# Kernel optimization log

Hardware: AMD Instinct MI355X
Metric: run time of the kernel (lower is better)

## Reference

```python
import jax, jax.numpy as jnp
import numpy as np

GRID = 128          # grid_size n
C_MARKERS = 32      # marker embed dim C
M_RHS = 64          # number of right-hand sides m
LENGTH_SCALE = 5.0  # spatial Matern length scale
KERNEL_JITTER = 0.01
MARKER_JITTER = 0.01


def _matern15_eigh(n, length_scale):
    # 1D Matern nu=1.5 kernel on linspace(0,1,n), eigendecomposed (as in __init__)
    x = np.linspace(0.0, 1.0, n)
    d = np.abs(x[:, None] - x[None, :]) / length_scale
    s3d = np.sqrt(3.0) * d
    K = (1.0 + s3d) * np.exp(-s3d)
    lam, V = np.linalg.eigh(K)
    return lam.astype(np.float32), V.astype(np.float32)


def setup_inputs() -> dict:
    key = jax.random.key(0)
    k_v, k_e = jax.random.split(key)
    n, C, m = GRID, C_MARKERS, M_RHS

    lam, V = _matern15_eigh(n, LENGTH_SCALE)

    # Marker covariance K_C = E E^T + marker_jitter * I, eigendecomposed
    E = np.asarray(jax.random.normal(k_e, (C, C), dtype=jnp.float32))
    K_C = E @ E.T + MARKER_JITTER * np.eye(C, dtype=np.float32)
    lam_C, V_C = np.linalg.eigh(K_C)

    # triple_eigs[i,j,k] = lam[i]*lam[j]*lam_C[k] + kernel_jitter  (all > 0)
    triple_eigs = (lam[:, None, None] * lam[None, :, None] * lam_C[None, None, :]
                   + KERNEL_JITTER).astype(np.float32)

    v = jax.random.normal(k_v, (n * n * C, m), dtype=jnp.float32)
    return {
        "v": v,
        "V_C": jnp.asarray(V_C.astype(np.float32)),
        "V": jnp.asarray(V),
        "triple_eigs": jnp.asarray(triple_eigs),
    }


def reference(v, V_C, V, triple_eigs):
    """A^{-1} v via triple-Kronecker eigenbasis: 3 forward rotations,
    eigenvalue divide, 3 reverse rotations. v: [n*n*C, m]."""
    n = V.shape[0]
    C = V_C.shape[0]
    m = v.shape[-1]
    V3 = v.reshape(n, n, C, m)
    tmp = jnp.einsum('ijcm,ck->ijkm', V3, V_C)     # rotate marker axis
    tmp = jnp.einsum('ijkm,jb->ibkm', tmp, V)      # rotate spatial y
    tmp = jnp.einsum('ibkm,ia->abkm', tmp, V)      # rotate spatial x
    tmp = tmp / triple_eigs[..., None]             # divide by eigenvalues
    tmp = jnp.einsum('abkm,jb->ajkm', tmp, V)      # un-rotate spatial y
    tmp = jnp.einsum('ajkm,ia->ijkm', tmp, V)      # un-rotate spatial x
    tmp = jnp.einsum('ijkm,ck->ijcm', tmp, V_C)    # un-rotate marker axis
    return tmp.reshape(n * n * C, m)
```

## Files before the change

kernel.cpp:

```cpp
#include <hip/hip_runtime.h>
#include <stdint.h>


typedef unsigned short ushort_t;
typedef __attribute__((ext_vector_type(8))) short short8;
typedef __attribute__((ext_vector_type(4))) float f32x4;

__device__ __forceinline__ ushort_t f2bf(float f) {
  union { float f; uint32_t u; } v; v.f = f;
  uint32_t u = v.u;
  return (ushort_t)((u + 0x7fffu + ((u >> 16) & 1u)) >> 16);
}
__device__ __forceinline__ uint32_t pk2(float a, float b) {
  return (uint32_t)f2bf(a) | ((uint32_t)f2bf(b) << 16);
}
__device__ __forceinline__ float bf2f(ushort_t u) {
  union { uint32_t x; float f; } v; v.x = (uint32_t)u << 16; return v.f;
}

__global__ __launch_bounds__(256) void prep_kernel(
    const float* __restrict__ te, const float* __restrict__ Vg,
    float* __restrict__ rte, ushort_t* __restrict__ Vhg, ushort_t* __restrict__ Vtg) {
  int b = blockIdx.x, t = threadIdx.x;
  if (b < 256) {
    int id = b * 256 + t;
    int o0 = id * 8;
    int k = o0 >> 14, ab0 = o0 & 16383;
    float r[8];
    #pragma unroll
    for (int e = 0; e < 8; ++e) r[e] = 1.0f / te[(ab0 + e) * 32 + k];
    *(float4*)(rte + o0)     = make_float4(r[0], r[1], r[2], r[3]);
    *(float4*)(rte + o0 + 4) = make_float4(r[4], r[5], r[6], r[7]);
  } else {
    int base = (b - 256) * 4096 + t;
    #pragma unroll
    for (int e = 0; e < 16; ++e) {
      int idx = base + e * 256;
      ushort_t us = f2bf(Vg[idx]);
      Vhg[idx] = us;
      Vtg[(idx & 127) * 128 + (idx >> 7)] = us;
    }
  }
}

__global__ __launch_bounds__(256) void k1_rot_t(
    const float* __restrict__ v, const float* __restrict__ VC, ushort_t* __restrict__ W) {
  __shared__ ushort_t Xs[32 * 520];
  __shared__ ushort_t Wt[512 * 32];
  __shared__ float VCs[1024];
  int t = threadIdx.x, bid = blockIdx.x;
  int jc = bid >> 2, mt = bid & 3;
  int ji0 = jc * 32, mm0 = mt * 16;

  #pragma unroll
  for (int e = 0; e < 4; ++e) VCs[e * 256 + t] = VC[e * 256 + t];

  #pragma unroll
  for (int e = 0; e < 4; ++e) {
    int q = e * 256 + t;
    int jj = q >> 5, c = q & 31;
    const float* src = v + (size_t)(ji0 + jj) * 2048 + c * 64 + mm0;
    float4 f0 = *(const float4*)(src);
    float4 f1 = *(const float4*)(src + 4);
    float4 f2 = *(const float4*)(src + 8);
    float4 f3 = *(const float4*)(src + 12);
    uint4 lo = make_uint4(pk2(f0.x, f0.y), pk2(f0.z, f0.w), pk2(f1.x, f1.y), pk2(f1.z, f1.w));
    uint4 hi = make_uint4(pk2(f2.x, f2.y), pk2(f2.z, f2.w), pk2(f3.x, f3.y), pk2(f3.z, f3.w));
    ushort_t* dst = &Xs[jj * 520 + c * 16];
    *(uint4*)dst = lo;
    *(uint4*)(dst + 8) = hi;
  }
  __syncthreads();

  int jj = t & 31, kq = t >> 5;
  float acc[4][16];
  #pragma unroll
  for (int e = 0; e < 4; ++e)
    #pragma unroll
    for (int q = 0; q < 16; ++q) acc[e][q] = 0.f;

  for (int c = 0; c < 32; ++c) {
    const ushort_t* xp = &Xs[jj * 520 + c * 16];
    short8 x0 = *(const short8*)xp;
    short8 x1 = *(const short8*)(xp + 8);
    float vc0 = VCs[c * 32 + kq * 4 + 0];
    float vc1 = VCs[c * 32 + kq * 4 + 1];
    float vc2 = VCs[c * 32 + kq * 4 + 2];
    float vc3 = VCs[c * 32 + kq * 4 + 3];
    #pragma unroll
    for (int q = 0; q < 8; ++q) {
      float xf = bf2f((ushort_t)x0[q]);
      acc[0][q] += vc0 * xf; acc[1][q] += vc1 * xf;
      acc[2][q] += vc2 * xf; acc[3][q] += vc3 * xf;
    }
    #pragma unroll
    for (int q = 0; q < 8; ++q) {
      float xf = bf2f((ushort_t)x1[q]);
      acc[0][8 + q] += vc0 * xf; acc[1][8 + q] += vc1 * xf;
      acc[2][8 + q] += vc2 * xf; acc[3][8 + q] += vc3 * xf;
    }
  }

  #pragma unroll
  for (int e = 0; e < 4; ++e)
    #pragma unroll
    for (int q = 0; q < 16; ++q)
      Wt[((kq * 4 + e) * 16 + q) * 32 + jj] = f2bf(acc[e][q]);
  __syncthreads();

  int part = t & 3, rq = t >> 2;
  #pragma unroll
  for (int e = 0; e < 8; ++e) {
    int row = e * 64 + rq;
    int k = row >> 4, mmi = row & 15;
    uint4 d = *(const uint4*)&Wt[row * 32 + part * 8];
    *(uint4*)(W + (size_t)(k * 64 + mm0 + mmi) * 16384 + ji0 + part * 8) = d;
  }
}

__device__ __forceinline__ void gemm128(const ushort_t (*__restrict__ Am)[136],
                                        const ushort_t (*__restrict__ Bm)[136],
                                        int r0, int c0, int lr, int lk, f32x4 acc[2][4]) {
  #pragma unroll
  for (int fr = 0; fr < 2; ++fr)
    #pragma unroll
    for (int fc = 0; fc < 4; ++fc) acc[fr][fc] = (f32x4){0.f, 0.f, 0.f, 0.f};
  #pragma unroll
  for (int kb = 0; kb < 4; ++kb) {
    short8 a[2], b[4];
    #pragma unroll
    for (int fr = 0; fr < 2; ++fr)
      a[fr] = *(const short8*)&Am[r0 + fr * 16 + lr][kb * 32 + lk];
    #pragma unroll
    for (int fc = 0; fc < 4; ++fc)
      b[fc] = *(const short8*)&Bm[c0 + fc * 16 + lr][kb * 32 + lk];
    #pragma unroll
    for (int fr = 0; fr < 2; ++fr)
      #pragma unroll
      for (int fc = 0; fc < 4; ++fc)
        acc[fr][fc] = __builtin_amdgcn_mfma_f32_16x16x32_bf16(a[fr], b[fc], acc[fr][fc], 0, 0, 0);
  }
}

__global__ __launch_bounds__(512, 2) void k3_chain(
    const ushort_t* __restrict__ W, const ushort_t* __restrict__ Vhg,
    const ushort_t* __restrict__ Vtg, const float* __restrict__ rte,
    ushort_t* __restrict__ U) {
  __shared__ ushort_t Ab[128][136];
  __shared__ ushort_t Vb[128][136];
  int t = threadIdx.x;
  int blk = blockIdx.x;
  int kk = blk >> 6;

  {
    const uint4* Wp = (const uint4*)W + (size_t)blk * 2048;
    const uint4* Vp = (const uint4*)Vtg;
    #pragma unroll
    for (int e = 0; e < 4; ++e) {
      int idx = e * 512 + t;
      int row = idx >> 4, part = idx & 15;
      *(uint4*)&Ab[row][part * 8] = Wp[idx];
      *(uint4*)&Vb[row][part * 8] = Vp[idx];
    }
  }
  __syncthreads();

  int wave = t >> 6, lane = t & 63;
  int r0 = (wave >> 1) * 32, c0 = (wave & 1) * 64;
  int lr = lane & 15;
  int lk = (lane >> 4) * 8;
  int rowreg = (lane >> 4) * 4;

  f32x4 acc[2][4];

  gemm128(Vb, Ab, r0, c0, lr, lk, acc);
  __syncthreads();
  #pragma unroll
  for (int fr = 0; fr < 2; ++fr)
    #pragma unroll
    for (int fc = 0; fc < 4; ++fc)
      #pragma unroll
      for (int r = 0; r < 4; ++r)
        Ab[r0 + fr * 16 + rowreg + r][c0 + fc * 16 + lr] = f2bf(acc[fr][fc][r]);
  __syncthreads();

  gemm128(Ab, Vb, r0, c0, lr, lk, acc);
  #pragma unroll
  for (int fr = 0; fr < 2; ++fr)
    #pragma unroll
    for (int fc = 0; fc < 4; ++fc)
      #pragma unroll
      for (int r = 0; r < 4; ++r) {
        int a = r0 + fr * 16 + rowreg + r;
        int bcol = c0 + fc * 16 + lr;
        acc[fr][fc][r] *= rte[(size_t)kk * 16384 + a * 128 + bcol];
      }
  __syncthreads();
  #pragma unroll
  for (int fr = 0; fr < 2; ++fr)
    #pragma unroll
    for (int fc = 0; fc < 4; ++fc) {
      int bcol = c0 + fc * 16 + lr;
      int abase = r0 + fr * 16 + rowreg;
      uint32_t lo = (uint32_t)f2bf(acc[fr][fc][0]) | ((uint32_t)f2bf(acc[fr][fc][1]) << 16);
      uint32_t hi = (uint32_t)f2bf(acc[fr][fc][2]) | ((uint32_t)f2bf(acc[fr][fc][3]) << 16);
      *(uint2*)&Ab[bcol][abase] = make_uint2(lo, hi);
    }
  {
    const uint4* Vp = (const uint4*)Vhg;
    #pragma unroll
    for (int e = 0; e < 4; ++e) {
      int idx = e * 512 + t;
      int row = idx >> 4, part = idx & 15;
      *(uint4*)&Vb[row][part * 8] = Vp[idx];
    }
  }
  __syncthreads();

  gemm128(Vb, Ab, r0, c0, lr, lk, acc);
  __syncthreads();
  #pragma unroll
  for (int fr = 0; fr < 2; ++fr)
    #pragma unroll
    for (int fc = 0; fc < 4; ++fc)
      #pragma unroll
      for (int r = 0; r < 4; ++r)
        Ab[r0 + fr * 16 + rowreg + r][c0 + fc * 16 + lr] = f2bf(acc[fr][fc][r]);
  __syncthreads();

  gemm128(Ab, Vb, r0, c0, lr, lk, acc);
  __syncthreads();
  #pragma unroll
  for (int fr = 0; fr < 2; ++fr)
    #pragma unroll
    for (int fc = 0; fc < 4; ++fc)
      #pragma unroll
      for (int r = 0; r < 4; ++r)
        Ab[r0 + fr * 16 + rowreg + r][c0 + fc * 16 + lr] = f2bf(acc[fr][fc][r]);
  __syncthreads();

  {
    const size_t ub = (size_t)blk * 16384;
    #pragma unroll
    for (int e = 0; e < 4; ++e) {
      int idx = e * 512 + t;
      int row = idx >> 4, part = idx & 15;
      *(uint4*)(U + ub + row * 128 + part * 8) = *(const uint4*)&Ab[row][part * 8];
    }
  }
}

__global__ __launch_bounds__(256) void k5_unrot_t(
    const ushort_t* __restrict__ U, const float* __restrict__ VC, float* __restrict__ out) {
  __shared__ ushort_t Us[512 * 40];
  __shared__ float VCs[1024];
  int t = threadIdx.x, bid = blockIdx.x;
  int jc = bid >> 2, mt = bid & 3;
  int jip0 = jc * 32, mm0 = mt * 16;

  #pragma unroll
  for (int e = 0; e < 4; ++e) VCs[e * 256 + t] = VC[e * 256 + t];

  #pragma unroll
  for (int e = 0; e < 2; ++e) {
    int row = e * 256 + t;
    int k = row >> 4, mmi = row & 15;
    const uint4* src = (const uint4*)(U + (size_t)(k * 64 + mm0 + mmi) * 16384 + jip0);
    ushort_t* dst = &Us[row * 40];
    *(uint4*)(dst)      = src[0];
    *(uint4*)(dst + 8)  = src[1];
    *(uint4*)(dst + 16) = src[2];
    *(uint4*)(dst + 24) = src[3];
  }
  __syncthreads();

  int jj = t & 31, cq = t >> 5;
  float acc[4][16];
  #pragma unroll
  for (int e = 0; e < 4; ++e)
    #pragma unroll
    for (int q = 0; q < 16; ++q) acc[e][q] = 0.f;

  for (int k = 0; k < 32; ++k) {
    float y[16];
    #pragma unroll
    for (int q = 0; q < 16; ++q)
      y[q] = bf2f(Us[(k * 16 + q) * 40 + jj]);
    float vc0 = VCs[(cq * 4 + 0) * 32 + k];
    float vc1 = VCs[(cq * 4 + 1) * 32 + k];
    float vc2 = VCs[(cq * 4 + 2) * 32 + k];
    float vc3 = VCs[(cq * 4 + 3) * 32 + k];
    #pragma unroll
    for (int q = 0; q < 16; ++q) {
      acc[0][q] += vc0 * y[q]; acc[1][q] += vc1 * y[q];
      acc[2][q] += vc2 * y[q]; acc[3][q] += vc3 * y[q];
    }
  }

  int i = ((jc & 3) << 5) + jj;
  int j = jc >> 2;
  float* ob = out + ((size_t)(i * 128 + j) * 32) * 64 + mm0;
  #pragma unroll
  for (int e = 0; e < 4; ++e) {
    float* oc = ob + (size_t)(cq * 4 + e) * 64;
    *(float4*)(oc)      = make_float4(acc[e][0],  acc[e][1],  acc[e][2],  acc[e][3]);
    *(float4*)(oc + 4)  = make_float4(acc[e][4],  acc[e][5],  acc[e][6],  acc[e][7]);
    *(float4*)(oc + 8)  = make_float4(acc[e][8],  acc[e][9],  acc[e][10], acc[e][11]);
    *(float4*)(oc + 12) = make_float4(acc[e][12], acc[e][13], acc[e][14], acc[e][15]);
  }
}

extern "C" void kernel_launch(void* const* d_in, const int* in_sizes, int n_in,
                              void* d_out, int out_size, void* d_ws, size_t ws_size,
                              hipStream_t stream) {
  (void)in_sizes; (void)n_in; (void)out_size; (void)ws_size;
  const float* v  = (const float*)d_in[0];
  const float* VC = (const float*)d_in[1];
  const float* Vg = (const float*)d_in[2];
  const float* te = (const float*)d_in[3];
  float* out = (float*)d_out;

  char* ws = (char*)d_ws;
  ushort_t* W   = (ushort_t*)(ws);
  ushort_t* U   = (ushort_t*)(ws + 67108864);
  float*    rte = (float*)   (ws + 134217728);
  ushort_t* Vhg = (ushort_t*)(ws + 136314880);
  ushort_t* Vtg = (ushort_t*)(ws + 136347648);

  prep_kernel<<<260, 256, 0, stream>>>(te, Vg, rte, Vhg, Vtg);
  k1_rot_t<<<2048, 256, 0, stream>>>(v, VC, W);
  k3_chain<<<2048, 512, 0, stream>>>(W, Vhg, Vtg, rte, U);
  k5_unrot_t<<<2048, 256, 0, stream>>>(U, VC, out);
}
```

Baseline: 400.4 us.

## Cut LDS footprint, read V operands from global, pack FMA math

k3_chain no longer stages V/V^T in shared memory. It reads the A/B MFMA fragments straight from global (L2-resident) memory and writes U directly from registers, which drops the second LDS buffer and lets launch bounds request more resident blocks. k1 and k5 switch to packed float2 FMAs with paired bf16 unpacking, and they reuse or shrink LDS buffers to raise occupancy. The risk is that global fragment loads in the inner MFMA loop bring more latency and uncoalesced traffic than the LDS staging they replace.

```diff
diff --git a/kernel.cpp b/kernel.cpp
--- a/kernel.cpp
+++ b/kernel.cpp
@@ -5,6 +5,7 @@
 typedef unsigned short ushort_t;
 typedef __attribute__((ext_vector_type(8))) short short8;
 typedef __attribute__((ext_vector_type(4))) float f32x4;
+typedef __attribute__((ext_vector_type(2))) float f32x2;
 
 __device__ __forceinline__ ushort_t f2bf(float f) {
   union { float f; uint32_t u; } v; v.f = f;
@@ -14,8 +15,11 @@
 __device__ __forceinline__ uint32_t pk2(float a, float b) {
   return (uint32_t)f2bf(a) | ((uint32_t)f2bf(b) << 16);
 }
-__device__ __forceinline__ float bf2f(ushort_t u) {
-  union { uint32_t x; float f; } v; v.x = (uint32_t)u << 16; return v.f;
+__device__ __forceinline__ float bf_lo(uint32_t w) {
+  union { uint32_t u; float f; } v; v.u = w << 16; return v.f;
+}
+__device__ __forceinline__ float bf_hi(uint32_t w) {
+  union { uint32_t u; float f; } v; v.u = w & 0xffff0000u; return v.f;
 }
 
 __global__ __launch_bounds__(256) void prep_kernel(
@@ -43,10 +47,9 @@
   }
 }
 
-__global__ __launch_bounds__(256) void k1_rot_t(
+__global__ __launch_bounds__(256, 4) void k1_rot_t(
     const float* __restrict__ v, const float* __restrict__ VC, ushort_t* __restrict__ W) {
-  __shared__ ushort_t Xs[32 * 520];
-  __shared__ ushort_t Wt[512 * 32];
+  __shared__ ushort_t S[16640];
   __shared__ float VCs[1024];
   int t = threadIdx.x, bid = blockIdx.x;
   int jc = bid >> 2, mt = bid & 3;
@@ -66,46 +69,47 @@
     float4 f3 = *(const float4*)(src + 12);
     uint4 lo = make_uint4(pk2(f0.x, f0.y), pk2(f0.z, f0.w), pk2(f1.x, f1.y), pk2(f1.z, f1.w));
     uint4 hi = make_uint4(pk2(f2.x, f2.y), pk2(f2.z, f2.w), pk2(f3.x, f3.y), pk2(f3.z, f3.w));
-    ushort_t* dst = &Xs[jj * 520 + c * 16];
+    ushort_t* dst = &S[jj * 520 + c * 16];
     *(uint4*)dst = lo;
     *(uint4*)(dst + 8) = hi;
   }
   __syncthreads();
 
   int jj = t & 31, kq = t >> 5;
-  float acc[4][16];
+  f32x2 acc2[4][8];
   #pragma unroll
   for (int e = 0; e < 4; ++e)
     #pragma unroll
-    for (int q = 0; q < 16; ++q) acc[e][q] = 0.f;
+    for (int q = 0; q < 8; ++q) acc2[e][q] = (f32x2){0.f, 0.f};
 
   for (int c = 0; c < 32; ++c) {
-    const ushort_t* xp = &Xs[jj * 520 + c * 16];
-    short8 x0 = *(const short8*)xp;
-    short8 x1 = *(const short8*)(xp + 8);
-    float vc0 = VCs[c * 32 + kq * 4 + 0];
-    float vc1 = VCs[c * 32 + kq * 4 + 1];
-    float vc2 = VCs[c * 32 + kq * 4 + 2];
-    float vc3 = VCs[c * 32 + kq * 4 + 3];
+    const uint32_t* xp = (const uint32_t*)&S[jj * 520 + c * 16];
+    uint4 wa = *(const uint4*)xp;
+    uint4 wb = *(const uint4*)(xp + 4);
+    uint32_t w[8] = {wa.x, wa.y, wa.z, wa.w, wb.x, wb.y, wb.z, wb.w};
+    f32x2 vc2[4];
+    #pragma unroll
+    for (int e = 0; e < 4; ++e) {
+      float s = VCs[c * 32 + kq * 4 + e];
+      vc2[e] = (f32x2){s, s};
+    }
     #pragma unroll
     for (int q = 0; q < 8; ++q) {
-      float xf = bf2f((ushort_t)x0[q]);
-      acc[0][q] += vc0 * xf; acc[1][q] += vc1 * xf;
-      acc[2][q] += vc2 * xf; acc[3][q] += vc3 * xf;
-    }
+      f32x2 x2 = (f32x2){bf_lo(w[q]), bf_hi(w[q])};
+      #pragma unroll
+      for (int e = 0; e < 4; ++e) acc2[e][q] += vc2[e] * x2;
+    }
+  }
+  __syncthreads();
+
+  #pragma unroll
+  for (int e = 0; e < 4; ++e)
     #pragma unroll
     for (int q = 0; q < 8; ++q) {
-      float xf = bf2f((ushort_t)x1[q]);
-      acc[0][8 + q] += vc0 * xf; acc[1][8 + q] += vc1 * xf;
-      acc[2][8 + q] += vc2 * xf; acc[3][8 + q] += vc3 * xf;
-    }
-  }
-
-  #pragma unroll
-  for (int e = 0; e < 4; ++e)
-    #pragma unroll
-    for (int q = 0; q < 16; ++q)
-      Wt[((kq * 4 + e) * 16 + q) * 32 + jj] = f2bf(acc[e][q]);
+      int row = (kq * 4 + e) * 16 + 2 * q;
+      S[row * 32 + jj]       = f2bf(acc2[e][q].x);
+      S[(row + 1) * 32 + jj] = f2bf(acc2[e][q].y);
+    }
   __syncthreads();
 
   int part = t & 3, rq = t >> 2;
@@ -113,14 +117,14 @@
   for (int e = 0; e < 8; ++e) {
     int row = e * 64 + rq;
     int k = row >> 4, mmi = row & 15;
-    uint4 d = *(const uint4*)&Wt[row * 32 + part * 8];
+    uint4 d = *(const uint4*)&S[row * 32 + part * 8];
     *(uint4*)(W + (size_t)(k * 64 + mm0 + mmi) * 16384 + ji0 + part * 8) = d;
   }
 }
 
-__device__ __forceinline__ void gemm128(const ushort_t (*__restrict__ Am)[136],
-                                        const ushort_t (*__restrict__ Bm)[136],
-                                        int r0, int c0, int lr, int lk, f32x4 acc[2][4]) {
+__device__ __forceinline__ void gemmGA(const ushort_t* __restrict__ Vg,
+                                       const ushort_t (*__restrict__ Bm)[136],
+                                       int r0, int c0, int lr, int lk, f32x4 acc[2][4]) {
   #pragma unroll
   for (int fr = 0; fr < 2; ++fr)
     #pragma unroll
@@ -130,7 +134,7 @@
     short8 a[2], b[4];
     #pragma unroll
     for (int fr = 0; fr < 2; ++fr)
-      a[fr] = *(const short8*)&Am[r0 + fr * 16 + lr][kb * 32 + lk];
+      a[fr] = *(const short8*)(Vg + (r0 + fr * 16 + lr) * 128 + kb * 32 + lk);
     #pragma unroll
     for (int fc = 0; fc < 4; ++fc)
       b[fc] = *(const short8*)&Bm[c0 + fc * 16 + lr][kb * 32 + lk];
@@ -141,26 +145,46 @@
         acc[fr][fc] = __builtin_amdgcn_mfma_f32_16x16x32_bf16(a[fr], b[fc], acc[fr][fc], 0, 0, 0);
   }
 }
-
-__global__ __launch_bounds__(512, 2) void k3_chain(
+__device__ __forceinline__ void gemmGB(const ushort_t (*__restrict__ Am)[136],
+                                       const ushort_t* __restrict__ Vg,
+                                       int r0, int c0, int lr, int lk, f32x4 acc[2][4]) {
+  #pragma unroll
+  for (int fr = 0; fr < 2; ++fr)
+    #pragma unroll
+    for (int fc = 0; fc < 4; ++fc) acc[fr][fc] = (f32x4){0.f, 0.f, 0.f, 0.f};
+  #pragma unroll
+  for (int kb = 0; kb < 4; ++kb) {
+    short8 a[2], b[4];
+    #pragma unroll
+    for (int fr = 0; fr < 2; ++fr)
+      a[fr] = *(const short8*)&Am[r0 + fr * 16 + lr][kb * 32 + lk];
+    #pragma unroll
+    for (int fc = 0; fc < 4; ++fc)
+      b[fc] = *(const short8*)(Vg + (c0 + fc * 16 + lr) * 128 + kb * 32 + lk);
+    #pragma unroll
+    for (int fr = 0; fr < 2; ++fr)
+      #pragma unroll
+      for (int fc = 0; fc < 4; ++fc)
+        acc[fr][fc] = __builtin_amdgcn_mfma_f32_16x16x32_bf16(a[fr], b[fc], acc[fr][fc], 0, 0, 0);
+  }
+}
+
+__global__ __launch_bounds__(512, 6) void k3_chain(
     const ushort_t* __restrict__ W, const ushort_t* __restrict__ Vhg,
     const ushort_t* __restrict__ Vtg, const float* __restrict__ rte,
     ushort_t* __restrict__ U) {
   __shared__ ushort_t Ab[128][136];
-  __shared__ ushort_t Vb[128][136];
   int t = threadIdx.x;
   int blk = blockIdx.x;
   int kk = blk >> 6;
 
   {
     const uint4* Wp = (const uint4*)W + (size_t)blk * 2048;
-    const uint4* Vp = (const uint4*)Vtg;
     #pragma unroll
     for (int e = 0; e < 4; ++e) {
       int idx = e * 512 + t;
       int row = idx >> 4, part = idx & 15;
       *(uint4*)&Ab[row][part * 8] = Wp[idx];
-      *(uint4*)&Vb[row][part * 8] = Vp[idx];
     }
   }
   __syncthreads();
@@ -173,7 +197,7 @@
 
   f32x4 acc[2][4];
 
-  gemm128(Vb, Ab, r0, c0, lr, lk, acc);
+  gemmGA(Vtg, Ab, r0, c0, lr, lk, acc);
   __syncthreads();
   #pragma unroll
   for (int fr = 0; fr < 2; ++fr)
@@ -184,7 +208,7 @@
         Ab[r0 + fr * 16 + rowreg + r][c0 + fc * 16 + lr] = f2bf(acc[fr][fc][r]);
   __syncthreads();
 
-  gemm128(Ab, Vb, r0, c0, lr, lk, acc);
+  gemmGB(Ab, Vtg, r0, c0, lr, lk, acc);
   #pragma unroll
   for (int fr = 0; fr < 2; ++fr)
     #pragma unroll
@@ -206,18 +230,9 @@
       uint32_t hi = (uint32_t)f2bf(acc[fr][fc][2]) | ((uint32_t)f2bf(acc[fr][fc][3]) << 16);
       *(uint2*)&Ab[bcol][abase] = make_uint2(lo, hi);
     }
-  {
-    const uint4* Vp = (const uint4*)Vhg;
-    #pragma unroll
-    for (int e = 0; e < 4; ++e) {
-      int idx = e * 512 + t;
-      int row = idx >> 4, part = idx & 15;
-      *(uint4*)&Vb[row][part * 8] = Vp[idx];
-    }
-  }
-  __syncthreads();
-
-  gemm128(Vb, Ab, r0, c0, lr, lk, acc);
+  __syncthreads();
+
+  gemmGA(Vhg, Ab, r0, c0, lr, lk, acc);
   __syncthreads();
   #pragma unroll
   for (int fr = 0; fr < 2; ++fr)
@@ -228,31 +243,20 @@
         Ab[r0 + fr * 16 + rowreg + r][c0 + fc * 16 + lr] = f2bf(acc[fr][fc][r]);
   __syncthreads();
 
-  gemm128(Ab, Vb, r0, c0, lr, lk, acc);
-  __syncthreads();
+  gemmGB(Ab, Vhg, r0, c0, lr, lk, acc);
+  ushort_t* Ub = U + (size_t)blk * 16384;
   #pragma unroll
   for (int fr = 0; fr < 2; ++fr)
     #pragma unroll
     for (int fc = 0; fc < 4; ++fc)
       #pragma unroll
       for (int r = 0; r < 4; ++r)
-        Ab[r0 + fr * 16 + rowreg + r][c0 + fc * 16 + lr] = f2bf(acc[fr][fc][r]);
-  __syncthreads();
-
-  {
-    const size_t ub = (size_t)blk * 16384;
-    #pragma unroll
-    for (int e = 0; e < 4; ++e) {
-      int idx = e * 512 + t;
-      int row = idx >> 4, part = idx & 15;
-      *(uint4*)(U + ub + row * 128 + part * 8) = *(const uint4*)&Ab[row][part * 8];
-    }
-  }
-}
-
-__global__ __launch_bounds__(256) void k5_unrot_t(
+        Ub[(r0 + fr * 16 + rowreg + r) * 128 + (c0 + fc * 16 + lr)] = f2bf(acc[fr][fc][r]);
+}
+
+__global__ __launch_bounds__(256, 4) void k5_unrot_t(
     const ushort_t* __restrict__ U, const float* __restrict__ VC, float* __restrict__ out) {
-  __shared__ ushort_t Us[512 * 40];
+  __shared__ ushort_t Us[512 * 34];
   __shared__ float VCs[1024];
   int t = threadIdx.x, bid = blockIdx.x;
   int jc = bid >> 2, mt = bid & 3;
@@ -266,47 +270,49 @@
     int row = e * 256 + t;
     int k = row >> 4, mmi = row & 15;
     const uint4* src = (const uint4*)(U + (size_t)(k * 64 + mm0 + mmi) * 16384 + jip0);
-    ushort_t* dst = &Us[row * 40];
-    *(uint4*)(dst)      = src[0];
-    *(uint4*)(dst + 8)  = src[1];
-    *(uint4*)(dst + 16) = src[2];
-    *(uint4*)(dst + 24) = src[3];
-  }
-  __syncthreads();
-
-  int jj = t & 31, cq = t >> 5;
-  float acc[4][16];
-  #pragma unroll
-  for (int e = 0; e < 4; ++e)
-    #pragma unroll
-    for (int q = 0; q < 16; ++q) acc[e][q] = 0.f;
+    uint4 d0 = src[0], d1 = src[1], d2 = src[2], d3 = src[3];
+    uint32_t* dst = (uint32_t*)&Us[row * 34];
+    dst[0] = d0.x;  dst[1] = d0.y;  dst[2]  = d0.z;  dst[3]  = d0.w;
+    dst[4] = d1.x;  dst[5] = d1.y;  dst[6]  = d1.z;  dst[7]  = d1.w;
+    dst[8] = d2.x;  dst[9] = d2.y;  dst[10] = d2.z;  dst[11] = d2.w;
+    dst[12] = d3.x; dst[13] = d3.y; dst[14] = d3.z;  dst[15] = d3.w;
+  }
+  __syncthreads();
+
+  int jj2 = t & 15, cq = t >> 4;
+  f32x2 acc2[2][16];
+  #pragma unroll
+  for (int e = 0; e < 2; ++e)
+    #pragma unroll
+    for (int q = 0; q < 16; ++q) acc2[e][q] = (f32x2){0.f, 0.f};
 
   for (int k = 0; k < 32; ++k) {
-    float y[16];
-    #pragma unroll
-    for (int q = 0; q < 16; ++q)
-      y[q] = bf2f(Us[(k * 16 + q) * 40 + jj]);
-    float vc0 = VCs[(cq * 4 + 0) * 32 + k];
-    float vc1 = VCs[(cq * 4 + 1) * 32 + k];
-    float vc2 = VCs[(cq * 4 + 2) * 32 + k];
-    float vc3 = VCs[(cq * 4 + 3) * 32 + k];
+    float s0 = VCs[(cq * 2 + 0) * 32 + k];
+    float s1 = VCs[(cq * 2 + 1) * 32 + k];
+    f32x2 v0 = (f32x2){s0, s0}, v1 = (f32x2){s1, s1};
     #pragma unroll
     for (int q = 0; q < 16; ++q) {
-      acc[0][q] += vc0 * y[q]; acc[1][q] += vc1 * y[q];
-      acc[2][q] += vc2 * y[q]; acc[3][q] += vc3 * y[q];
-    }
-  }
-
-  int i = ((jc & 3) << 5) + jj;
+      uint32_t w = *(const uint32_t*)&Us[(k * 16 + q) * 34 + 2 * jj2];
+      f32x2 y2 = (f32x2){bf_lo(w), bf_hi(w)};
+      acc2[0][q] += v0 * y2;
+      acc2[1][q] += v1 * y2;
+    }
+  }
+
+  int i = ((jc & 3) << 5) + 2 * jj2;
   int j = jc >> 2;
-  float* ob = out + ((size_t)(i * 128 + j) * 32) * 64 + mm0;
-  #pragma unroll
-  for (int e = 0; e < 4; ++e) {
-    float* oc = ob + (size_t)(cq * 4 + e) * 64;
-    *(float4*)(oc)      = make_float4(acc[e][0],  acc[e][1],  acc[e][2],  acc[e][3]);
-    *(float4*)(oc + 4)  = make_float4(acc[e][4],  acc[e][5],  acc[e][6],  acc[e][7]);
-    *(float4*)(oc + 8)  = make_float4(acc[e][8],  acc[e][9],  acc[e][10], acc[e][11]);
-    *(float4*)(oc + 12) = make_float4(acc[e][12], acc[e][13], acc[e][14], acc[e][15]);
+  #pragma unroll
+  for (int cc = 0; cc < 2; ++cc) {
+    int c = cq * 2 + cc;
+    float* o0 = out + (((size_t)i * 128 + j) * 32 + c) * 64 + mm0;
+    float* o1 = o0 + (size_t)128 * 32 * 64;
+    #pragma unroll
+    for (int z = 0; z < 4; ++z) {
+      *(float4*)(o0 + z * 4) = make_float4(acc2[cc][z * 4 + 0].x, acc2[cc][z * 4 + 1].x,
+                                           acc2[cc][z * 4 + 2].x, acc2[cc][z * 4 + 3].x);
+      *(float4*)(o1 + z * 4) = make_float4(acc2[cc][z * 4 + 0].y, acc2[cc][z * 4 + 1].y,
+                                           acc2[cc][z * 4 + 2].y, acc2[cc][z * 4 + 3].y);
+    }
   }
 }
 
```

Measured after the change: 504.6 us. +26.0%, slower.
